# Performance work log

Hardware: AMD Instinct MI355X
Metric: run time of the kernel (lower is better)

## Reference

```python
import jax, jax.numpy as jnp
import numpy as np

B, T, C, H = 2, 2048, 1024, 16
D = C // H  # head dim = 64

def setup_inputs() -> dict:
    key = jax.random.key(0)
    ks = jax.random.split(key, 5)
    s = 0.02
    return {
        "x": jax.random.normal(ks[0], (B, T, C), dtype=jnp.float32),
        "Wqkv": jax.random.normal(ks[1], (C, 3 * C), dtype=jnp.float32) * s,
        "bqkv": jnp.zeros((3 * C,), dtype=jnp.float32),
        "Wproj": jax.random.normal(ks[2], (C, C), dtype=jnp.float32) * s,
        "bproj": jnp.zeros((C,), dtype=jnp.float32),
    }

def reference(x, Wqkv, bqkv, Wproj, bproj):
    b, t, c = x.shape
    qkv = x @ Wqkv + bqkv                       # [B,T,3C]
    q, k, v = jnp.split(qkv, 3, axis=-1)
    # [B,T,C] -> [B,H,T,D]
    q = q.reshape(b, t, H, D).transpose(0, 2, 1, 3)
    k = k.reshape(b, t, H, D).transpose(0, 2, 1, 3)
    v = v.reshape(b, t, H, D).transpose(0, 2, 1, 3)
    scale = 1.0 / np.sqrt(D).astype(np.float32)
    attn = jnp.einsum('bhqd,bhkd->bhqk', q, k) * scale  # [B,H,T,T]
    causal = jnp.tril(jnp.ones((t, t), dtype=bool))
    attn = jnp.where(causal, attn, jnp.float32(-jnp.inf))
    attn = jax.nn.softmax(attn, axis=-1)
    y = jnp.einsum('bhqk,bhkd->bhqd', attn, v)          # [B,H,T,D]
    y = y.transpose(0, 2, 1, 3).reshape(b, t, c)        # [B,T,C]
    return y @ Wproj + bproj
```

## Files before the change

kernel.cpp:

```cpp
#include <hip/hip_runtime.h>
#include <stdint.h>

#define B_ 2
#define T_ 2048
#define C_ 1024
#define H_ 16
#define D_ 64
#define M_ (B_*T_)
#define BHTD_ (B_*H_*T_*D_)

#define AS1 __attribute__((address_space(1)))
#define AS3 __attribute__((address_space(3)))

typedef __bf16 bf16x8 __attribute__((ext_vector_type(8)));
typedef __bf16 bf16x4 __attribute__((ext_vector_type(4)));
typedef float f32x4 __attribute__((ext_vector_type(4)));

static __device__ __forceinline__ unsigned short f32_bf16(float f) {
    unsigned int u = __float_as_uint(f);
    u += 0x7FFFu + ((u >> 16) & 1u);
    return (unsigned short)(u >> 16);
}

__global__ void prep_kernel(const float* __restrict__ x, unsigned short* __restrict__ xbf,
                            const float* __restrict__ Wqkv, unsigned short* __restrict__ wqkv_t,
                            const float* __restrict__ Wproj, unsigned short* __restrict__ wproj_t) {
    __shared__ float tile[32][33];
    const int id = blockIdx.x;
    const int tid = threadIdx.x;
    if (id < 2048) {
        int i = (id * 256 + tid) * 8;
        float4 f0 = *(const float4*)(x + i);
        float4 f1 = *(const float4*)(x + i + 4);
        ushort4 o0, o1;
        o0.x = f32_bf16(f0.x); o0.y = f32_bf16(f0.y); o0.z = f32_bf16(f0.z); o0.w = f32_bf16(f0.w);
        o1.x = f32_bf16(f1.x); o1.y = f32_bf16(f1.y); o1.z = f32_bf16(f1.z); o1.w = f32_bf16(f1.w);
        uint4 w;
        w.x = __builtin_bit_cast(unsigned int, *(ushort2*)&o0.x);
        w.y = __builtin_bit_cast(unsigned int, *(ushort2*)&o0.z);
        w.z = __builtin_bit_cast(unsigned int, *(ushort2*)&o1.x);
        w.w = __builtin_bit_cast(unsigned int, *(ushort2*)&o1.z);
        *(uint4*)(xbf + i) = w;
        return;
    }
    const float* W; unsigned short* Wt; int K, N, bx, by;
    if (id < 5120) {
        int r = id - 2048; W = Wqkv; Wt = wqkv_t; K = 1024; N = 3072;
        bx = r % 96; by = r / 96;
    } else {
        int r = id - 5120; W = Wproj; Wt = wproj_t; K = 1024; N = 1024;
        bx = r & 31; by = r >> 5;
    }
    int n0 = bx * 32, k0 = by * 32;
    int tx = tid & 31, ty = tid >> 5;
    #pragma unroll
    for (int j = 0; j < 32; j += 8)
        tile[ty + j][tx] = W[(size_t)(k0 + ty + j) * N + n0 + tx];
    __syncthreads();
    #pragma unroll
    for (int j = 0; j < 32; j += 8)
        Wt[(size_t)(n0 + ty + j) * K + k0 + tx] = f32_bf16(tile[tx][ty + j]);
}

template<int EPI, int BN>
__global__ __launch_bounds__(256) void gemm_bt(
    const unsigned short* __restrict__ A,
    const unsigned short* __restrict__ Bt,
    const float* __restrict__ bias,
    unsigned short* __restrict__ out_bf16,
    float* __restrict__ out_f32,
    int M, int N, int K)
{
    constexpr int NI = (BN == 128) ? 4 : 2;
    constexpr int BSTR = BN * 32;
    __shared__ __align__(16) unsigned short smem[16640];
    unsigned short* AsU = smem;
    unsigned short* BsU = smem + 8192;
    int tid = threadIdx.x;
    int lane = tid & 63, wid = tid >> 6;
    int fr = lane & 15, fg = lane >> 4;
    int row0 = blockIdx.x * 128, col0 = blockIdx.y * BN;
    int wm = (wid >> 1) * 64, wn = (wid & 1) * (BN / 2);

    f32x4 acc[4][NI];
    #pragma unroll
    for (int i = 0; i < 4; ++i)
        #pragma unroll
        for (int j = 0; j < NI; ++j)
            acc[i][j] = (f32x4){0.f, 0.f, 0.f, 0.f};

    const int srw = lane >> 2;
    const int scl = (lane & 3) * 8;
    const int c0 = wid * 2, c1 = wid * 2 + 1;

    auto stage = [&](int buf, int k0) {
        __builtin_amdgcn_global_load_lds(
            (const AS1 void*)(A + (size_t)(row0 + c0 * 16 + srw) * K + k0 + scl),
            (AS3 void*)(AsU + buf * 4096 + c0 * 512), 16, 0, 0);
        __builtin_amdgcn_global_load_lds(
            (const AS1 void*)(A + (size_t)(row0 + c1 * 16 + srw) * K + k0 + scl),
            (AS3 void*)(AsU + buf * 4096 + c1 * 512), 16, 0, 0);
        if (BN == 128) {
            __builtin_amdgcn_global_load_lds(
                (const AS1 void*)(Bt + (size_t)(col0 + c0 * 16 + srw) * K + k0 + scl),
                (AS3 void*)(BsU + buf * BSTR + c0 * 512), 16, 0, 0);
            __builtin_amdgcn_global_load_lds(
                (const AS1 void*)(Bt + (size_t)(col0 + c1 * 16 + srw) * K + k0 + scl),
                (AS3 void*)(BsU + buf * BSTR + c1 * 512), 16, 0, 0);
        } else {
            __builtin_amdgcn_global_load_lds(
                (const AS1 void*)(Bt + (size_t)(col0 + wid * 16 + srw) * K + k0 + scl),
                (AS3 void*)(BsU + buf * BSTR + wid * 512), 16, 0, 0);
        }
    };

    stage(0, 0);
    __syncthreads();

    int cur = 0;
    for (int k0 = 0; k0 < K; k0 += 32) {
        if (k0 + 32 < K) stage(cur ^ 1, k0 + 32);

        bf16x8 af[4], bfr[NI];
        #pragma unroll
        for (int i = 0; i < 4; ++i)
            af[i] = *(const bf16x8*)(AsU + cur * 4096 + (wm + i * 16 + fr) * 32 + fg * 8);
        #pragma unroll
        for (int i = 0; i < NI; ++i)
            bfr[i] = *(const bf16x8*)(BsU + cur * BSTR + (wn + i * 16 + fr) * 32 + fg * 8);
        #pragma unroll
        for (int mi = 0; mi < 4; ++mi)
            #pragma unroll
            for (int ni = 0; ni < NI; ++ni)
                acc[mi][ni] = __builtin_amdgcn_mfma_f32_16x16x32_bf16(af[mi], bfr[ni], acc[mi][ni], 0, 0, 0);

        __syncthreads();
        cur ^= 1;
    }

    if (EPI == 0 && col0 >= 2048) {
        #pragma unroll
        for (int ni = 0; ni < NI; ++ni) {
            const int cl = wn + ni * 16 + fr;
            const float bv = bias[col0 + cl];
            #pragma unroll
            for (int mi = 0; mi < 4; ++mi) {
                const int rl = wm + mi * 16 + fg * 4;
                bf16x4 pk = {(__bf16)(acc[mi][ni][0] + bv), (__bf16)(acc[mi][ni][1] + bv),
                             (__bf16)(acc[mi][ni][2] + bv), (__bf16)(acc[mi][ni][3] + bv)};
                uint2 w = __builtin_bit_cast(uint2, pk);
                *(unsigned int*)(smem + cl * 130 + rl)     = w.x;
                *(unsigned int*)(smem + cl * 130 + rl + 2) = w.y;
            }
        }
        __syncthreads();
        constexpr int TPC = 256 / BN;
        constexpr int SEG = 128 / TPC;
        const int c = tid / TPC, seg = tid % TPC;
        const int col = col0 + c;
        const int d = col & 63, h2 = (col >> 6) & 15;
        const int bb = row0 >> 11;
        const int t0 = (row0 & 2047) + seg * SEG;
        unsigned short* dst = out_bf16 + (size_t)2 * BHTD_ +
                              ((size_t)(bb * H_ + h2) * D_ + d) * T_ + t0;
        const unsigned short* src = smem + c * 130 + seg * SEG;
        #pragma unroll
        for (int j = 0; j < SEG / 8; ++j) {
            uint4 v;
            v.x = *(const unsigned int*)(src + j * 8 + 0);
            v.y = *(const unsigned int*)(src + j * 8 + 2);
            v.z = *(const unsigned int*)(src + j * 8 + 4);
            v.w = *(const unsigned int*)(src + j * 8 + 6);
            *(uint4*)(dst + j * 8) = v;
        }
        return;
    }

    #pragma unroll
    for (int mi = 0; mi < 4; ++mi) {
        int rowb = row0 + wm + mi * 16 + fg * 4;
        #pragma unroll
        for (int ni = 0; ni < NI; ++ni) {
            int col = col0 + wn + ni * 16 + fr;
            float bv = bias[col];
            #pragma unroll
            for (int r = 0; r < 4; ++r) {
                float v = acc[mi][ni][r] + bv;
                int rr = rowb + r;
                if (EPI == 0) {
                    int part = col >> 10, c = col & 1023;
                    int h = c >> 6, d = c & 63;
                    int b = rr >> 11, t = rr & 2047;
                    if (part == 0) v *= 0.18033688011112042f;
                    size_t idx = (size_t)part * BHTD_ + ((size_t)(b * H_ + h) * T_ + t) * D_ + d;
                    out_bf16[idx] = f32_bf16(v);
                } else {
                    out_f32[(size_t)rr * N + col] = v;
                }
            }
        }
    }
}

__global__ __launch_bounds__(256) void attn_kernel(
    const unsigned short* __restrict__ qg,
    const unsigned short* __restrict__ kg,
    const unsigned short* __restrict__ vtg,
    unsigned short* __restrict__ y)
{
    const int id = blockIdx.x;
    const int xcd = id & 7, loc = id >> 3;
    const int bh = xcd * 4 + (loc & 3);
    const int iq0 = loc >> 2;
    const int iq = (iq0 < 8) ? iq0 : 23 - iq0;
    const int chlo = iq, chhi = 31 - iq;
    const int b = bh >> 4, h = bh & 15;
    const int tid = threadIdx.x, wid = tid >> 6, lane = tid & 63;
    const int fr = lane & 15, fg = lane >> 4;

    const unsigned short* qp = qg + (size_t)bh * (T_ * D_);
    const char* kpB = (const char*)(kg + (size_t)bh * (T_ * D_));
    const char* vpB = (const char*)(vtg + (size_t)bh * (D_ * T_));

    __shared__ __align__(16) char Ks[2][8192];
    __shared__ __align__(16) char Vs[2][8192];
    __shared__ __align__(16) char Ps[4][32 * 128];
    char* Pw = Ps[wid];

    const int rhi = chhi * 64 + wid * 16;
    const int rlo = chlo * 64 + wid * 16;

    bf16x8 qhi[2], qlo[2];
    #pragma unroll
    for (int kd = 0; kd < 2; ++kd) {
        qhi[kd] = *(const bf16x8*)(qp + (size_t)(rhi + fr) * D_ + kd * 32 + fg * 8);
        qlo[kd] = *(const bf16x8*)(qp + (size_t)(rlo + fr) * D_ + kd * 32 + fg * 8);
    }

    f32x4 oHi[4], oLo[4];
    float lHi = 0.f, lLo = 0.f;
    #pragma unroll
    for (int n = 0; n < 4; ++n) {
        oHi[n] = (f32x4){0.f, 0.f, 0.f, 0.f};
        oLo[n] = (f32x4){0.f, 0.f, 0.f, 0.f};
    }

    const int ntk  = chhi + 1;
    const int ntlo = chlo + 1;

    const int srow8 = lane >> 3;
    const int scol  = (lane & 7) * 16;
    const int ssw   = srow8 << 4;

    auto stage = [&](int buf, int kv0) {
        #pragma unroll
        for (int bc = 0; bc < 2; ++bc) {
            const int rbase = wid * 16 + bc * 8;
            __builtin_amdgcn_global_load_lds(
                (const AS1 void*)(kpB + (size_t)(kv0 + rbase + srow8) * 128 + (scol ^ ssw)),
                (AS3 void*)(Ks[buf] + rbase * 128), 16, 0, 0);
            __builtin_amdgcn_global_load_lds(
                (const AS1 void*)(vpB + (size_t)(rbase + srow8) * 4096 + (size_t)kv0 * 2 + (scol ^ ssw)),
                (AS3 void*)(Vs[buf] + rbase * 128), 16, 0, 0);
        }
    };

    stage(0, 0);
    __syncthreads();

    const unsigned lsw = (unsigned)((fr & 7) << 4);
    int cur = 0;
    for (int t = 0; t < ntk; ++t) {
        const int kv0 = t * 64;
        if (t + 1 < ntk) stage(cur ^ 1, kv0 + 64);

        const char* Kb = Ks[cur];
        const char* Vb = Vs[cur];
        const bool lo_act = (t < ntlo);

        f32x4 sh[4], sl[4];
        #pragma unroll
        for (int n = 0; n < 4; ++n) {
            sh[n] = (f32x4){0.f, 0.f, 0.f, 0.f};
            sl[n] = (f32x4){0.f, 0.f, 0.f, 0.f};
        }
        __builtin_amdgcn_s_setprio(1);
        #pragma unroll
        for (int kd = 0; kd < 2; ++kd)
            #pragma unroll
            for (int n = 0; n < 4; ++n) {
                bf16x8 kf = *(const bf16x8*)(Kb + (n * 16 + fr) * 128 +
                                             (((unsigned)(kd * 64 + fg * 16)) ^ lsw));
                sh[n] = __builtin_amdgcn_mfma_f32_16x16x32_bf16(kf, qhi[kd], sh[n], 0, 0, 0);
                if (lo_act)
                    sl[n] = __builtin_amdgcn_mfma_f32_16x16x32_bf16(kf, qlo[kd], sl[n], 0, 0, 0);
            }
        __builtin_amdgcn_s_setprio(0);

        bf16x8 vf[4][2];
        #pragma unroll
        for (int nd = 0; nd < 4; ++nd)
            #pragma unroll
            for (int kk = 0; kk < 2; ++kk)
                vf[nd][kk] = *(const bf16x8*)(Vb + (nd * 16 + fr) * 128 +
                                              (((unsigned)(kk * 64 + fg * 16)) ^ lsw));

        {
            const bool masked = (t == chhi);
            const int qrow = rhi + fr;
            const unsigned prow = (unsigned)fr * 128;
            #pragma unroll
            for (int n = 0; n < 4; ++n) {
                float x0 = sh[n][0], x1 = sh[n][1], x2 = sh[n][2], x3 = sh[n][3];
                if (masked) {
                    const int kvb = kv0 + n * 16 + fg * 4;
                    if (kvb     > qrow) x0 = -1e30f;
                    if (kvb + 1 > qrow) x1 = -1e30f;
                    if (kvb + 2 > qrow) x2 = -1e30f;
                    if (kvb + 3 > qrow) x3 = -1e30f;
                }
                const float p0 = __builtin_amdgcn_exp2f(x0);
                const float p1 = __builtin_amdgcn_exp2f(x1);
                const float p2 = __builtin_amdgcn_exp2f(x2);
                const float p3 = __builtin_amdgcn_exp2f(x3);
                lHi += (p0 + p1) + (p2 + p3);
                bf16x4 pk4 = {(__bf16)p0, (__bf16)p1, (__bf16)p2, (__bf16)p3};
                *(uint2*)(Pw + ((prow + (unsigned)(n * 32 + fg * 8)) ^ lsw)) =
                    __builtin_bit_cast(uint2, pk4);
            }
        }
        {
            const unsigned prow = (unsigned)fr * 128;
            __builtin_amdgcn_s_setprio(1);
            #pragma unroll
            for (int kk = 0; kk < 2; ++kk) {
                bf16x8 pb = *(const bf16x8*)(Pw + ((prow + (unsigned)(kk * 64 + fg * 16)) ^ lsw));
                #pragma unroll
                for (int nd = 0; nd < 4; ++nd)
                    oHi[nd] = __builtin_amdgcn_mfma_f32_16x16x32_bf16(vf[nd][kk], pb, oHi[nd], 0, 0, 0);
            }
            __builtin_amdgcn_s_setprio(0);
        }
        if (lo_act) {
            const bool masked = (t == chlo);
            const int qrow = rlo + fr;
            const unsigned prow = (unsigned)(16 + fr) * 128;
            #pragma unroll
            for (int n = 0; n < 4; ++n) {
                float x0 = sl[n][0], x1 = sl[n][1], x2 = sl[n][2], x3 = sl[n][3];
                if (masked) {
                    const int kvb = kv0 + n * 16 + fg * 4;
                    if (kvb     > qrow) x0 = -1e30f;
                    if (kvb + 1 > qrow) x1 = -1e30f;
                    if (kvb + 2 > qrow) x2 = -1e30f;
                    if (kvb + 3 > qrow) x3 = -1e30f;
                }
                const float p0 = __builtin_amdgcn_exp2f(x0);
                const float p1 = __builtin_amdgcn_exp2f(x1);
                const float p2 = __builtin_amdgcn_exp2f(x2);
                const float p3 = __builtin_amdgcn_exp2f(x3);
                lLo += (p0 + p1) + (p2 + p3);
                bf16x4 pk4 = {(__bf16)p0, (__bf16)p1, (__bf16)p2, (__bf16)p3};
                *(uint2*)(Pw + ((prow + (unsigned)(n * 32 + fg * 8)) ^ lsw)) =
                    __builtin_bit_cast(uint2, pk4);
            }
            __builtin_amdgcn_s_setprio(1);
            #pragma unroll
            for (int kk = 0; kk < 2; ++kk) {
                bf16x8 pb = *(const bf16x8*)(Pw + ((prow + (unsigned)(kk * 64 + fg * 16)) ^ lsw));
                #pragma unroll
                for (int nd = 0; nd < 4; ++nd)
                    oLo[nd] = __builtin_amdgcn_mfma_f32_16x16x32_bf16(vf[nd][kk], pb, oLo[nd], 0, 0, 0);
            }
            __builtin_amdgcn_s_setprio(0);
        }

        __syncthreads();
        cur ^= 1;
    }

    #pragma unroll
    for (int s = 0; s < 2; ++s) {
        float rs = s ? lLo : lHi;
        rs += __shfl_xor(rs, 16);
        rs += __shfl_xor(rs, 32);
        const float inv = 1.f / rs;
        const int trow = (s ? rlo : rhi) + fr;
        f32x4* oT = s ? oLo : oHi;
        #pragma unroll
        for (int nd = 0; nd < 4; ++nd) {
            bf16x4 ov = {(__bf16)(oT[nd][0] * inv), (__bf16)(oT[nd][1] * inv),
                         (__bf16)(oT[nd][2] * inv), (__bf16)(oT[nd][3] * inv)};
            *(uint2*)(y + ((size_t)b * T_ + trow) * C_ + h * 64 + nd * 16 + fg * 4) =
                __builtin_bit_cast(uint2, ov);
        }
    }
}

extern "C" void kernel_launch(void* const* d_in, const int* in_sizes, int n_in,
                              void* d_out, int out_size, void* d_ws, size_t ws_size,
                              hipStream_t stream) {
    const float* x     = (const float*)d_in[0];
    const float* Wqkv  = (const float*)d_in[1];
    const float* bqkv  = (const float*)d_in[2];
    const float* Wproj = (const float*)d_in[3];
    const float* bproj = (const float*)d_in[4];
    float* out = (float*)d_out;

    char* ws = (char*)d_ws;
    unsigned short* x_bf    = (unsigned short*)(ws);
    unsigned short* wqkv_t  = (unsigned short*)(ws + 8388608);
    unsigned short* wproj_t = (unsigned short*)(ws + 14680064);
    unsigned short* qkv     = (unsigned short*)(ws + 16777216);
    unsigned short* ybuf    = (unsigned short*)(ws + 41943040);

    prep_kernel<<<dim3(6144), 256, 0, stream>>>(x, x_bf, Wqkv, wqkv_t, Wproj, wproj_t);

    gemm_bt<0, 64><<<dim3(M_ / 128, 3072 / 64), 256, 0, stream>>>(
        x_bf, wqkv_t, bqkv, qkv, nullptr, M_, 3072, 1024);

    attn_kernel<<<dim3(512), 256, 0, stream>>>(
        qkv, qkv + (size_t)BHTD_, qkv + 2 * (size_t)BHTD_, ybuf);

    gemm_bt<1, 64><<<dim3(M_ / 128, 1024 / 64), 256, 0, stream>>>(
        ybuf, wproj_t, bproj, nullptr, out, M_, 1024, 1024);
}
```

Baseline: 116.2 us.

## Specialize QKV GEMM with 256x256 tiles, swizzled LDS and deeper pipelining

```diff
diff --git a/kernel.cpp b/kernel.cpp
--- a/kernel.cpp
+++ b/kernel.cpp
@@ -62,16 +62,157 @@
         Wt[(size_t)(n0 + ty + j) * K + k0 + tx] = f32_bf16(tile[tx][ty + j]);
 }
 
-template<int EPI, int BN>
-__global__ __launch_bounds__(256) void gemm_bt(
+__global__ __launch_bounds__(512, 1) void gemm_qkv(
     const unsigned short* __restrict__ A,
     const unsigned short* __restrict__ Bt,
     const float* __restrict__ bias,
-    unsigned short* __restrict__ out_bf16,
+    unsigned short* __restrict__ out_bf16)
+{
+    __shared__ __align__(16) char LDS[131072];
+    const int tid = threadIdx.x;
+    const int lane = tid & 63, wid = tid >> 6;
+    const int fr = lane & 15, fg = lane >> 4;
+    const int row0 = blockIdx.x * 256, col0 = blockIdx.y * 256;
+    const int wm = (wid >> 2) * 128;
+    const int wn = (wid & 3) * 64;
+
+    const char* Ab = (const char*)A;
+    const char* Bb = (const char*)Bt;
+
+    f32x4 acc[8][4];
+    #pragma unroll
+    for (int i = 0; i < 8; ++i)
+        #pragma unroll
+        for (int j = 0; j < 4; ++j)
+            acc[i][j] = (f32x4){0.f, 0.f, 0.f, 0.f};
+
+    const int sR0 = tid >> 2;
+    const int sC0 = (tid & 3) * 16;
+    auto stage = [&](int slot, int kt) {
+        char* base = LDS + slot * 32768;
+        const size_t koff = (size_t)kt * 64;
+        #pragma unroll
+        for (int j = 0; j < 2; ++j) {
+            const int R = j * 128 + sR0;
+            const int colb = sC0 ^ ((R & 3) << 4);
+            __builtin_amdgcn_global_load_lds(
+                (const AS1 void*)(Ab + (size_t)(row0 + R) * 2048 + koff + colb),
+                (AS3 void*)(base + j * 8192 + wid * 1024), 16, 0, 0);
+            __builtin_amdgcn_global_load_lds(
+                (const AS1 void*)(Bb + (size_t)(col0 + R) * 2048 + koff + colb),
+                (AS3 void*)(base + 16384 + j * 8192 + wid * 1024), 16, 0, 0);
+        }
+    };
+
+    const int nt = 32;
+    stage(0, 0);
+    stage(1, 1);
+    asm volatile("s_waitcnt vmcnt(4)\n\ts_barrier" ::: "memory");
+
+    const int swz = (fr & 3) << 4;
+    for (int kt = 0; kt < nt; ++kt) {
+        const char* Ak = LDS + (kt & 3) * 32768;
+        const char* Bk = Ak + 16384;
+        if (kt + 2 < nt) stage((kt + 2) & 3, kt + 2);
+
+        bf16x8 bfr[4];
+        #pragma unroll
+        for (int ni = 0; ni < 4; ++ni)
+            bfr[ni] = *(const bf16x8*)(Bk + (wn + ni * 16 + fr) * 64 + ((fg * 16) ^ swz));
+
+        #pragma unroll
+        for (int q = 0; q < 4; ++q) {
+            bf16x8 a0 = *(const bf16x8*)(Ak + (wm + (2 * q) * 16 + fr) * 64 + ((fg * 16) ^ swz));
+            bf16x8 a1 = *(const bf16x8*)(Ak + (wm + (2 * q + 1) * 16 + fr) * 64 + ((fg * 16) ^ swz));
+            __builtin_amdgcn_s_setprio(1);
+            #pragma unroll
+            for (int ni = 0; ni < 4; ++ni) {
+                acc[2 * q][ni]     = __builtin_amdgcn_mfma_f32_16x16x32_bf16(a0, bfr[ni], acc[2 * q][ni], 0, 0, 0);
+                acc[2 * q + 1][ni] = __builtin_amdgcn_mfma_f32_16x16x32_bf16(a1, bfr[ni], acc[2 * q + 1][ni], 0, 0, 0);
+            }
+            __builtin_amdgcn_s_setprio(0);
+        }
+
+        if (kt + 2 < nt)
+            asm volatile("s_waitcnt vmcnt(4)\n\ts_barrier" ::: "memory");
+        else if (kt + 1 < nt)
+            asm volatile("s_waitcnt vmcnt(0)\n\ts_barrier" ::: "memory");
+    }
+
+    const int part = col0 >> 10;
+    const int bb = row0 >> 11;
+
+    if (part < 2) {
+        const float qscale = (part == 0) ? 0.18033688011112042f : 1.0f;
+        #pragma unroll
+        for (int mi = 0; mi < 8; ++mi) {
+            const int rr = row0 + wm + mi * 16 + fg * 4;
+            const int t = rr & 2047;
+            #pragma unroll
+            for (int ni = 0; ni < 4; ++ni) {
+                const int col = col0 + wn + ni * 16 + fr;
+                const float bv = bias[col];
+                const int c = col & 1023, h = c >> 6, d = c & 63;
+                unsigned short* dst = out_bf16 + (size_t)part * BHTD_ +
+                                      ((size_t)(bb * H_ + h) * T_) * D_ + d;
+                #pragma unroll
+                for (int r = 0; r < 4; ++r)
+                    dst[(size_t)(t + r) * D_] = f32_bf16((acc[mi][ni][r] + bv) * qscale);
+            }
+        }
+        return;
+    }
+
+    __syncthreads();
+    unsigned short* tbuf = (unsigned short*)LDS;
+    #pragma unroll
+    for (int hc = 0; hc < 2; ++hc) {
+        if (((wid & 3) >> 1) == hc) {
+            #pragma unroll
+            for (int ni = 0; ni < 4; ++ni) {
+                const int cl = (wn - hc * 128) + ni * 16 + fr;
+                const float bv = bias[col0 + hc * 128 + cl];
+                #pragma unroll
+                for (int mi = 0; mi < 8; ++mi) {
+                    const int rl = wm + mi * 16 + fg * 4;
+                    bf16x4 pk = {(__bf16)(acc[mi][ni][0] + bv), (__bf16)(acc[mi][ni][1] + bv),
+                                 (__bf16)(acc[mi][ni][2] + bv), (__bf16)(acc[mi][ni][3] + bv)};
+                    uint2 w = __builtin_bit_cast(uint2, pk);
+                    *(unsigned int*)(tbuf + cl * 258 + rl)     = w.x;
+                    *(unsigned int*)(tbuf + cl * 258 + rl + 2) = w.y;
+                }
+            }
+        }
+        __syncthreads();
+        const int c = tid >> 2, seg = tid & 3;
+        const int col = col0 + hc * 128 + c;
+        const int d = col & 63, h2 = (col >> 6) & 15;
+        const int t0 = (row0 & 2047) + seg * 64;
+        unsigned short* dst = out_bf16 + (size_t)2 * BHTD_ +
+                              ((size_t)(bb * H_ + h2) * D_ + d) * T_ + t0;
+        const unsigned short* src = tbuf + c * 258 + seg * 64;
+        #pragma unroll
+        for (int j = 0; j < 8; ++j) {
+            uint4 v;
+            v.x = *(const unsigned int*)(src + j * 8 + 0);
+            v.y = *(const unsigned int*)(src + j * 8 + 2);
+            v.z = *(const unsigned int*)(src + j * 8 + 4);
+            v.w = *(const unsigned int*)(src + j * 8 + 6);
+            *(uint4*)(dst + j * 8) = v;
+        }
+        __syncthreads();
+    }
+}
+
+__global__ __launch_bounds__(256) void gemm_proj(
+    const unsigned short* __restrict__ A,
+    const unsigned short* __restrict__ Bt,
+    const float* __restrict__ bias,
     float* __restrict__ out_f32,
     int M, int N, int K)
 {
-    constexpr int NI = (BN == 128) ? 4 : 2;
+    constexpr int BN = 64;
+    constexpr int NI = 2;
     constexpr int BSTR = BN * 32;
     __shared__ __align__(16) unsigned short smem[16640];
     unsigned short* AsU = smem;
@@ -100,18 +241,9 @@
         __builtin_amdgcn_global_load_lds(
             (const AS1 void*)(A + (size_t)(row0 + c1 * 16 + srw) * K + k0 + scl),
             (AS3 void*)(AsU + buf * 4096 + c1 * 512), 16, 0, 0);
-        if (BN == 128) {
-            __builtin_amdgcn_global_load_lds(
-                (const AS1 void*)(Bt + (size_t)(col0 + c0 * 16 + srw) * K + k0 + scl),
-                (AS3 void*)(BsU + buf * BSTR + c0 * 512), 16, 0, 0);
-            __builtin_amdgcn_global_load_lds(
-                (const AS1 void*)(Bt + (size_t)(col0 + c1 * 16 + srw) * K + k0 + scl),
-                (AS3 void*)(BsU + buf * BSTR + c1 * 512), 16, 0, 0);
-        } else {
-            __builtin_amdgcn_global_load_lds(
-                (const AS1 void*)(Bt + (size_t)(col0 + wid * 16 + srw) * K + k0 + scl),
-                (AS3 void*)(BsU + buf * BSTR + wid * 512), 16, 0, 0);
-        }
+        __builtin_amdgcn_global_load_lds(
+            (const AS1 void*)(Bt + (size_t)(col0 + wid * 16 + srw) * K + k0 + scl),
+            (AS3 void*)(BsU + buf * BSTR + wid * 512), 16, 0, 0);
     };
 
     stage(0, 0);
@@ -138,44 +270,6 @@
         cur ^= 1;
     }
 
-    if (EPI == 0 && col0 >= 2048) {
-        #pragma unroll
-        for (int ni = 0; ni < NI; ++ni) {
-            const int cl = wn + ni * 16 + fr;
-            const float bv = bias[col0 + cl];
-            #pragma unroll
-            for (int mi = 0; mi < 4; ++mi) {
-                const int rl = wm + mi * 16 + fg * 4;
-                bf16x4 pk = {(__bf16)(acc[mi][ni][0] + bv), (__bf16)(acc[mi][ni][1] + bv),
-                             (__bf16)(acc[mi][ni][2] + bv), (__bf16)(acc[mi][ni][3] + bv)};
-                uint2 w = __builtin_bit_cast(uint2, pk);
-                *(unsigned int*)(smem + cl * 130 + rl)     = w.x;
-                *(unsigned int*)(smem + cl * 130 + rl + 2) = w.y;
-            }
-        }
-        __syncthreads();
-        constexpr int TPC = 256 / BN;
-        constexpr int SEG = 128 / TPC;
-        const int c = tid / TPC, seg = tid % TPC;
-        const int col = col0 + c;
-        const int d = col & 63, h2 = (col >> 6) & 15;
-        const int bb = row0 >> 11;
-        const int t0 = (row0 & 2047) + seg * SEG;
-        unsigned short* dst = out_bf16 + (size_t)2 * BHTD_ +
-                              ((size_t)(bb * H_ + h2) * D_ + d) * T_ + t0;
-        const unsigned short* src = smem + c * 130 + seg * SEG;
-        #pragma unroll
-        for (int j = 0; j < SEG / 8; ++j) {
-            uint4 v;
-            v.x = *(const unsigned int*)(src + j * 8 + 0);
-            v.y = *(const unsigned int*)(src + j * 8 + 2);
-            v.z = *(const unsigned int*)(src + j * 8 + 4);
-            v.w = *(const unsigned int*)(src + j * 8 + 6);
-            *(uint4*)(dst + j * 8) = v;
-        }
-        return;
-    }
-
     #pragma unroll
     for (int mi = 0; mi < 4; ++mi) {
         int rowb = row0 + wm + mi * 16 + fg * 4;
@@ -184,20 +278,8 @@
             int col = col0 + wn + ni * 16 + fr;
             float bv = bias[col];
             #pragma unroll
-            for (int r = 0; r < 4; ++r) {
-                float v = acc[mi][ni][r] + bv;
-                int rr = rowb + r;
-                if (EPI == 0) {
-                    int part = col >> 10, c = col & 1023;
-                    int h = c >> 6, d = c & 63;
-                    int b = rr >> 11, t = rr & 2047;
-                    if (part == 0) v *= 0.18033688011112042f;
-                    size_t idx = (size_t)part * BHTD_ + ((size_t)(b * H_ + h) * T_ + t) * D_ + d;
-                    out_bf16[idx] = f32_bf16(v);
-                } else {
-                    out_f32[(size_t)rr * N + col] = v;
-                }
-            }
+            for (int r = 0; r < 4; ++r)
+                out_f32[(size_t)(rowb + r) * N + col] = acc[mi][ni][r] + bv;
         }
     }
 }
@@ -416,12 +498,12 @@
 
     prep_kernel<<<dim3(6144), 256, 0, stream>>>(x, x_bf, Wqkv, wqkv_t, Wproj, wproj_t);
 
-    gemm_bt<0, 64><<<dim3(M_ / 128, 3072 / 64), 256, 0, stream>>>(
-        x_bf, wqkv_t, bqkv, qkv, nullptr, M_, 3072, 1024);
+    gemm_qkv<<<dim3(M_ / 256, 3072 / 256), 512, 0, stream>>>(
+        x_bf, wqkv_t, bqkv, qkv);
 
     attn_kernel<<<dim3(512), 256, 0, stream>>>(
         qkv, qkv + (size_t)BHTD_, qkv + 2 * (size_t)BHTD_, ybuf);
 
-    gemm_bt<1, 64><<<dim3(M_ / 128, 1024 / 64), 256, 0, stream>>>(
-        ybuf, wproj_t, bproj, nullptr, out, M_, 1024, 1024);
+    gemm_proj<<<dim3(M_ / 128, 1024 / 64), 256, 0, stream>>>(
+        ybuf, wproj_t, bproj, out, M_, 1024, 1024);
 }
```

Measured after the change: 113.2 us, median of 2. 2.5% less time.
